# Kernel optimization log

Hardware: AMD Instinct MI355X
Metric: run time of the kernel (lower is better)

Reference implementation:

```python
import jax, jax.numpy as jnp
import numpy as np

B, S, D, H, K = 16, 2048, 1024, 16, 31  # batch, seq, d_model, n_heads, kernel_size


def setup_inputs() -> dict:
    key = jax.random.key(0)
    ks = jax.random.split(key, 6)
    sc = 1.0 / np.sqrt(D)
    return {
        "query_sequences": jax.random.normal(ks[0], (B, S, D), jnp.float32),
        "key_sequences": jax.random.normal(ks[1], (B, S, D), jnp.float32),
        "value_sequences": jax.random.normal(ks[2], (B, S, D), jnp.float32),
        "key_value_sequence_lengths": jax.random.randint(ks[3], (B,), 1, S + 1, jnp.int32),
        "W_q": jax.random.normal(ks[4], (D, H * K), jnp.float32) * sc,  # cast_queries.weight^T
        "b_q": jnp.zeros((H * K,), jnp.float32),                        # cast_queries.bias
        "conv_bias": jnp.zeros((H,), jnp.float32),
    }


def reference(query_sequences, key_sequences, value_sequences,
              key_value_sequence_lengths, W_q, b_q, conv_bias):
    b, s, d = query_sequences.shape
    h = conv_bias.shape[0]
    k = W_q.shape[1] // h
    r = d // h
    # Generate per-position, per-head depthwise filters from the queries.
    weights = (query_sequences @ W_q + b_q).reshape(b, s, h, k)  # (B,S,H,K)
    # Split key channels into heads and reduce within each head -> (B,S,H)
    ksum = key_sequences.reshape(b, s, h, r).sum(axis=-1)
    pad_l = (k - 1) // 2
    pad_r = k - 1 - pad_l
    kpad = jnp.pad(ksum, ((0, 0), (pad_l, pad_r), (0, 0)))  # (B, S+K-1, H)
    # Cross-correlation with per-position filters:
    # out[b,t,h] = sum_j weights[b,t,h,j] * kpad[b, t+j, h]
    out = jnp.zeros((b, s, h), dtype=weights.dtype)
    for j in range(k):  # fixed small kernel loop
        out = out + weights[..., j] * kpad[:, j:j + s, :]
    out = out + conv_bias  # per-head bias
    return out.transpose(0, 2, 1)  # (B, n_heads, S)
```

## Files before the change

kernel.cpp:

```cpp
#include <hip/hip_runtime.h>
#include <hip/hip_bf16.h>

#define BB 16
#define SS 2048
#define DD 1024
#define HH 16
#define KK 31
#define HK 496

typedef float f32x4 __attribute__((ext_vector_type(4)));
typedef __bf16 bf16x8 __attribute__((ext_vector_type(8)));

__device__ __forceinline__ unsigned short f2bf(float x) {
  unsigned u = __float_as_uint(x);
  unsigned r = u + 0x7FFFu + ((u >> 16) & 1u);
  return (unsigned short)(r >> 16);
}

__global__ void prep_kernel(const float* __restrict__ Wq,
                            unsigned short* __restrict__ Bimg) {
  int idx = blockIdx.x * 256 + threadIdx.x;
  int e = idx & 7;
  int qq = (idx >> 3) & 15;
  int g = (idx >> 7) & 3;
  int n = (idx >> 9) & 3;
  int w = (idx >> 11) & 7;
  int ks = idx >> 14;
  int k = ks * 32 + g * 8 + e;
  int c = w * 64 + n * 16 + qq;
  int h = c >> 5, j = c & 31;
  float v = (j < KK) ? Wq[k * HK + h * KK + j] : 0.f;
  Bimg[idx] = f2bf(v);
}

__global__ void ksum_kernel(const float* __restrict__ key,
                            float* __restrict__ ksum) {
  const int row = blockIdx.x;
  const int tid = threadIdx.x;
  const float4 v = reinterpret_cast<const float4*>(key + (size_t)row * DD)[tid];
  float p = v.x + v.y + v.z + v.w;
  p += __shfl_xor(p, 1);
  p += __shfl_xor(p, 2);
  p += __shfl_xor(p, 4);
  p += __shfl_xor(p, 8);
  if ((tid & 15) == 0) ksum[(size_t)row * HH + (tid >> 4)] = p;
}

__global__ __launch_bounds__(512, 2) void mca_kernel(
    const float* __restrict__ q, const float* __restrict__ bq,
    const float* __restrict__ convb, const float* __restrict__ ksum,
    const unsigned short* __restrict__ Bimg, float* __restrict__ out) {
  extern __shared__ char smem[];
  const int tid = threadIdx.x;
  const int w = tid >> 6, lane = tid & 63;
  const int g = lane >> 4, qq = lane & 15;
  const int bid = blockIdx.x;
  const int bb = bid >> 5;
  const int t0 = (bid & 31) << 6;

  const float* qblk = q + ((size_t)(bb * SS + t0)) * DD;
  const unsigned short* bbase = Bimg + w * 2048 + lane * 8;

  f32x4 acc[4][4];
#pragma unroll
  for (int m = 0; m < 4; ++m)
#pragma unroll
    for (int n = 0; n < 4; ++n) acc[m][n] = (f32x4){0.f, 0.f, 0.f, 0.f};

#pragma unroll 8
  for (int it = 0; it < 32; ++it) {
    const int gidx = it * 512 + tid;
    const int row = gidx >> 8;
    const int c16 = gidx & 255;
    const float4 v = reinterpret_cast<const float4*>(qblk)[gidx];
    const int ks = c16 >> 3, gg = (c16 >> 1) & 3, half = c16 & 1;
    const unsigned u0 = (unsigned)f2bf(v.x) | ((unsigned)f2bf(v.y) << 16);
    const unsigned u1 = (unsigned)f2bf(v.z) | ((unsigned)f2bf(v.w) << 16);
    const int byte = (ks * 4096 + gg * 1024 + row * 16 + half * 8) ^ ((ks & 7) << 4);
    *reinterpret_cast<uint2*>(smem + byte) = make_uint2(u0, u1);
  }
  __syncthreads();

  auto loadB = [&](int ks, bf16x8* pB) {
    const unsigned short* p = bbase + (size_t)ks * 16384;
#pragma unroll
    for (int n = 0; n < 4; ++n)
      pB[n] = *reinterpret_cast<const bf16x8*>(p + n * 512);
  };
  auto compute = [&](int ks, const bf16x8* pB) {
    const int sw = (ks & 7) << 4;
    bf16x8 af[4];
#pragma unroll
    for (int m = 0; m < 4; ++m) {
      const int byte = (ks * 4096 + g * 1024 + (m * 16 + qq) * 16) ^ sw;
      af[m] = *reinterpret_cast<const bf16x8*>(smem + byte);
    }
#pragma unroll
    for (int m = 0; m < 4; ++m)
#pragma unroll
      for (int n = 0; n < 4; ++n)
        acc[m][n] = __builtin_amdgcn_mfma_f32_16x16x32_bf16(af[m], pB[n], acc[m][n], 0, 0, 0);
  };

  bf16x8 pBa[4], pBb[4];
  loadB(0, pBa);
#pragma unroll
  for (int k2 = 0; k2 < 16; ++k2) {
    loadB(2 * k2 + 1, pBb);
    compute(2 * k2, pBa);
    if (k2 < 15) loadB(2 * k2 + 2, pBa);
    compute(2 * k2 + 1, pBb);
  }

  float bqv[4];
#pragma unroll
  for (int n = 0; n < 4; ++n) {
    int c = w * 64 + n * 16 + qq;
    int h = c >> 5, j = c & 31;
    bqv[n] = (j < KK) ? bq[h * KK + j] : 0.f;
  }
  float cb[2] = {convb[w * 2], convb[w * 2 + 1]};

  __syncthreads();
  float* kl = reinterpret_cast<float*>(smem);
  for (int i = tid; i < 96 * 16; i += 512) {
    int trow = i >> 4, h = i & 15;
    int t = t0 + trow - 15;
    kl[trow * 17 + h] = (t >= 0 && t < SS) ? ksum[((size_t)bb * SS + t) * HH + h] : 0.f;
  }
  __syncthreads();

#pragma unroll
  for (int m = 0; m < 4; ++m) {
    float part[4][2];
#pragma unroll
    for (int r = 0; r < 4; ++r) {
      part[r][0] = 0.f;
      part[r][1] = 0.f;
    }
#pragma unroll
    for (int n = 0; n < 4; ++n) {
      const int hp = n >> 1;
      const int j = (n & 1) * 16 + qq;
      const int h = w * 2 + hp;
#pragma unroll
      for (int r = 0; r < 4; ++r) {
        const int tl = m * 16 + g * 4 + r;
        part[r][hp] += (acc[m][n][r] + bqv[n]) * kl[(tl + j) * 17 + h];
      }
    }
#pragma unroll
    for (int r = 0; r < 4; ++r)
#pragma unroll
      for (int hp = 0; hp < 2; ++hp) {
        float v = part[r][hp];
        v += __shfl_xor(v, 1);
        v += __shfl_xor(v, 2);
        v += __shfl_xor(v, 4);
        v += __shfl_xor(v, 8);
        part[r][hp] = v;
      }
    if (qq < 4) {
      const int r = qq;
      const int t = t0 + m * 16 + g * 4 + r;
#pragma unroll
      for (int hp = 0; hp < 2; ++hp)
        out[((size_t)bb * HH + w * 2 + hp) * SS + t] = part[r][hp] + cb[hp];
    }
  }
}

extern "C" void kernel_launch(void* const* d_in, const int* in_sizes, int n_in,
                              void* d_out, int out_size, void* d_ws, size_t ws_size,
                              hipStream_t stream) {
  const float* q   = (const float*)d_in[0];
  const float* key = (const float*)d_in[1];
  const float* Wq  = (const float*)d_in[4];
  const float* bq  = (const float*)d_in[5];
  const float* cvb = (const float*)d_in[6];
  float* out = (float*)d_out;

  float* ksum = (float*)d_ws;
  unsigned short* Bimg = (unsigned short*)((char*)d_ws + 2097152);

  hipFuncSetAttribute((const void*)mca_kernel,
                      hipFuncAttributeMaxDynamicSharedMemorySize, 131072);

  prep_kernel<<<2048, 256, 0, stream>>>(Wq, Bimg);
  ksum_kernel<<<BB * SS, 256, 0, stream>>>(key, ksum);
  mca_kernel<<<BB * (SS / 64), 512, 131072, stream>>>(q, bq, cvb, ksum, Bimg, out);
}
```

Baseline: 91.30 us.

## Split fused GEMM+conv into 128-row GEMM kernel and separate conv kernel

Replaces the fused mca kernel with a GEMM kernel that processes 128 query rows per block, loading K in two halves into LDS. Each block reuses the B-fragment loads across 8 M-tiles instead of 4, halving B traffic per row. The GEMM writes bf16 filter weights to workspace, and a separate conv kernel applies the per-position filter against ksum. This adds a write and read of a 32 MB bf16 intermediate plus an extra launch. The new path runs only when the workspace is large enough.

New measurement: 113.4 us. 1.24x slower.

```diff
diff --git a/kernel.cpp b/kernel.cpp
--- a/kernel.cpp
+++ b/kernel.cpp
@@ -11,10 +11,10 @@
 typedef float f32x4 __attribute__((ext_vector_type(4)));
 typedef __bf16 bf16x8 __attribute__((ext_vector_type(8)));
 
-__device__ __forceinline__ unsigned short f2bf(float x) {
+__device__ __forceinline__ unsigned f2bf(float x) {
   unsigned u = __float_as_uint(x);
   unsigned r = u + 0x7FFFu + ((u >> 16) & 1u);
-  return (unsigned short)(r >> 16);
+  return r >> 16;
 }
 
 __global__ void prep_kernel(const float* __restrict__ Wq,
@@ -30,7 +30,7 @@
   int c = w * 64 + n * 16 + qq;
   int h = c >> 5, j = c & 31;
   float v = (j < KK) ? Wq[k * HK + h * KK + j] : 0.f;
-  Bimg[idx] = f2bf(v);
+  Bimg[idx] = (unsigned short)f2bf(v);
 }
 
 __global__ void ksum_kernel(const float* __restrict__ key,
@@ -46,6 +46,131 @@
   if ((tid & 15) == 0) ksum[(size_t)row * HH + (tid >> 4)] = p;
 }
 
+__global__ __launch_bounds__(512, 2) void gemm_kernel(
+    const float* __restrict__ q, const float* __restrict__ bq,
+    const unsigned short* __restrict__ Bimg, unsigned short* __restrict__ wout) {
+  extern __shared__ char smem[];
+  const int tid = threadIdx.x;
+  const int w = tid >> 6, lane = tid & 63;
+  const int g = lane >> 4, qq = lane & 15;
+  const int bid = blockIdx.x;
+  const int bb = bid >> 4;
+  const int t0 = (bid & 15) << 7;
+
+  const float* qblk = q + ((size_t)(bb * SS + t0)) * DD;
+  const unsigned short* bbase = Bimg + w * 2048 + lane * 8;
+
+  f32x4 acc[8][4];
+#pragma unroll
+  for (int m = 0; m < 8; ++m)
+#pragma unroll
+    for (int n = 0; n < 4; ++n) acc[m][n] = (f32x4){0.f, 0.f, 0.f, 0.f};
+
+  auto loadB = [&](int ks, bf16x8* pB) {
+    const unsigned short* p = bbase + (size_t)ks * 16384;
+#pragma unroll
+    for (int n = 0; n < 4; ++n)
+      pB[n] = *reinterpret_cast<const bf16x8*>(p + n * 512);
+  };
+
+#pragma unroll
+  for (int hf = 0; hf < 2; ++hf) {
+    __syncthreads();
+#pragma unroll 8
+    for (int it = 0; it < 32; ++it) {
+      const int gidx = it * 512 + tid;
+      const int row = gidx >> 7;
+      const int c16 = gidx & 127;
+      const float4 v =
+          reinterpret_cast<const float4*>(qblk)[row * 256 + hf * 128 + c16];
+      const int ksl = c16 >> 3, gg = (c16 >> 1) & 3, h4 = c16 & 1;
+      const unsigned u0 = f2bf(v.x) | (f2bf(v.y) << 16);
+      const unsigned u1 = f2bf(v.z) | (f2bf(v.w) << 16);
+      const int byte =
+          (ksl * 8192 + gg * 2048 + row * 16 + h4 * 8) ^ ((ksl & 7) << 4);
+      *reinterpret_cast<uint2*>(smem + byte) = make_uint2(u0, u1);
+    }
+    __syncthreads();
+
+    bf16x8 pB0[4], pB1[4];
+    loadB(hf * 16, pB0);
+#pragma unroll
+    for (int ksl = 0; ksl < 16; ++ksl) {
+      bf16x8* cur = (ksl & 1) ? pB1 : pB0;
+      bf16x8* nxt = (ksl & 1) ? pB0 : pB1;
+      if (ksl < 15) loadB(hf * 16 + ksl + 1, nxt);
+      const int sw = (ksl & 7) << 4;
+      bf16x8 af[8];
+#pragma unroll
+      for (int m = 0; m < 8; ++m) {
+        const int byte = (ksl * 8192 + g * 2048 + (m * 16 + qq) * 16) ^ sw;
+        af[m] = *reinterpret_cast<const bf16x8*>(smem + byte);
+      }
+#pragma unroll
+      for (int m = 0; m < 8; ++m)
+#pragma unroll
+        for (int n = 0; n < 4; ++n)
+          acc[m][n] = __builtin_amdgcn_mfma_f32_16x16x32_bf16(af[m], cur[n],
+                                                              acc[m][n], 0, 0, 0);
+    }
+  }
+
+  float bqv[4];
+#pragma unroll
+  for (int n = 0; n < 4; ++n) {
+    int c = w * 64 + n * 16 + qq;
+    int h = c >> 5, j = c & 31;
+    bqv[n] = (j < KK) ? bq[h * KK + j] : 0.f;
+  }
+#pragma unroll
+  for (int m = 0; m < 8; ++m)
+#pragma unroll
+    for (int n = 0; n < 4; ++n)
+#pragma unroll
+      for (int r = 0; r < 4; ++r) {
+        const int t = t0 + m * 16 + g * 4 + r;
+        const int col = w * 64 + n * 16 + qq;
+        wout[(((size_t)(bb * SS + t)) << 9) + col] =
+            (unsigned short)f2bf(acc[m][n][r] + bqv[n]);
+      }
+}
+
+__global__ __launch_bounds__(512) void conv_kernel(
+    const unsigned short* __restrict__ wout, const float* __restrict__ ksum,
+    const float* __restrict__ convb, float* __restrict__ out) {
+  __shared__ float kl[160 * 17];
+  const int tid = threadIdx.x;
+  const int bid = blockIdx.x;
+  const int bb = bid >> 4;
+  const int t0 = (bid & 15) << 7;
+
+  for (int i = tid; i < 160 * 16; i += 512) {
+    int trow = i >> 4, h = i & 15;
+    int t = t0 + trow - 15;
+    kl[trow * 17 + h] = (t >= 0 && t < SS) ? ksum[((size_t)bb * SS + t) * HH + h] : 0.f;
+  }
+  __syncthreads();
+
+#pragma unroll
+  for (int it = 0; it < 4; ++it) {
+    const int i = it * 512 + tid;
+    const int h = i >> 7, row = i & 127;
+    const unsigned short* wp =
+        wout + (((size_t)(bb * SS + t0 + row)) << 9) + h * 32;
+    float s = 0.f;
+#pragma unroll
+    for (int u = 0; u < 4; ++u) {
+      bf16x8 wv = *reinterpret_cast<const bf16x8*>(wp + u * 8);
+#pragma unroll
+      for (int e = 0; e < 8; ++e) {
+        const int j = u * 8 + e;
+        s += (float)wv[e] * kl[(row + j) * 17 + h];
+      }
+    }
+    out[((size_t)(bb * HH + h)) * SS + t0 + row] = s + convb[h];
+  }
+}
+
 __global__ __launch_bounds__(512, 2) void mca_kernel(
     const float* __restrict__ q, const float* __restrict__ bq,
     const float* __restrict__ convb, const float* __restrict__ ksum,
@@ -74,8 +199,8 @@
     const int c16 = gidx & 255;
     const float4 v = reinterpret_cast<const float4*>(qblk)[gidx];
     const int ks = c16 >> 3, gg = (c16 >> 1) & 3, half = c16 & 1;
-    const unsigned u0 = (unsigned)f2bf(v.x) | ((unsigned)f2bf(v.y) << 16);
-    const unsigned u1 = (unsigned)f2bf(v.z) | ((unsigned)f2bf(v.w) << 16);
+    const unsigned u0 = f2bf(v.x) | (f2bf(v.y) << 16);
+    const unsigned u1 = f2bf(v.z) | (f2bf(v.w) << 16);
     const int byte = (ks * 4096 + gg * 1024 + row * 16 + half * 8) ^ ((ks & 7) << 4);
     *reinterpret_cast<uint2*>(smem + byte) = make_uint2(u0, u1);
   }
@@ -181,12 +306,20 @@
   float* out = (float*)d_out;
 
   float* ksum = (float*)d_ws;
-  unsigned short* Bimg = (unsigned short*)((char*)d_ws + 2097152);
-
-  hipFuncSetAttribute((const void*)mca_kernel,
-                      hipFuncAttributeMaxDynamicSharedMemorySize, 131072);
+  unsigned short* Bimg = (unsigned short*)((char*)d_ws + (2 << 20));
+  unsigned short* wout = (unsigned short*)((char*)d_ws + (3 << 20));
 
   prep_kernel<<<2048, 256, 0, stream>>>(Wq, Bimg);
   ksum_kernel<<<BB * SS, 256, 0, stream>>>(key, ksum);
-  mca_kernel<<<BB * (SS / 64), 512, 131072, stream>>>(q, bq, cvb, ksum, Bimg, out);
-}
+
+  if (ws_size >= (size_t)(36 << 20)) {
+    hipFuncSetAttribute((const void*)gemm_kernel,
+                        hipFuncAttributeMaxDynamicSharedMemorySize, 131072);
+    gemm_kernel<<<BB * (SS / 128), 512, 131072, stream>>>(q, bq, Bimg, wout);
+    conv_kernel<<<BB * (SS / 128), 512, 0, stream>>>(wout, ksum, cvb, out);
+  } else {
+    hipFuncSetAttribute((const void*)mca_kernel,
+                        hipFuncAttributeMaxDynamicSharedMemorySize, 131072);
+    mca_kernel<<<BB * (SS / 64), 512, 131072, stream>>>(q, bq, cvb, ksum, Bimg, out);
+  }
+}
```
